# Kernel tuning notes

Hardware: AMD Instinct MI355X
Metric: run time of the kernel (lower is better)

## Reference

```python
import jax, jax.numpy as jnp
import numpy as np

T, K = 2048, 6          # tokens, activated experts per token
DIM = 2048              # model dim
INTER = 1408            # moe intermediate dim
E = 16                  # routed experts (group_size, shared not fused)


def setup_inputs() -> dict:
    key = jax.random.key(0)
    k1, k2, k3, k4, k5, k6 = jax.random.split(key, 6)
    x = jax.random.normal(k1, (T, DIM), dtype=jnp.float32)
    weights = jax.random.uniform(k2, (T, K), dtype=jnp.float32)
    indices = jax.random.randint(k3, (T, K), 0, E, dtype=jnp.int64)
    s = 1.0 / np.sqrt(DIM)
    Wg = jax.random.normal(k4, (E, INTER, DIM), dtype=jnp.float32) * s
    Wu = jax.random.normal(k5, (E, INTER, DIM), dtype=jnp.float32) * s
    Wd = jax.random.normal(k6, (E, DIM, INTER), dtype=jnp.float32) * (1.0 / np.sqrt(INTER))
    return {"x": x, "weights": weights, "indices": indices,
            "Wg": Wg, "Wu": Wu, "Wd": Wd}


def reference(x, weights, indices, Wg, Wu, Wd):
    # per-token combine weight for each expert: [T, E]
    # gate_w[t, e] = sum_k weights[t, k] * (indices[t, k] == e)
    one_hot = jax.nn.one_hot(indices, E, dtype=x.dtype)        # [T, K, E]
    gate_w = jnp.einsum('tk,tke->te', weights, one_hot)        # [T, E]

    # SwiGLU expert FFN, dense over experts, combine folded pre-down-proj
    g = jnp.einsum('td,eid->tei', x, Wg)                       # [T, E, INTER]
    u = jnp.einsum('td,eid->tei', x, Wu)                       # [T, E, INTER]
    act = jax.nn.silu(g) * u                                   # [T, E, INTER]
    # y[t] = sum_e gate_w[t,e] * (act[t,e] @ Wd[e].T)
    y = jnp.einsum('tei,edi->td', act * gate_w[:, :, None], Wd)  # [T, DIM]
    return y
```

## Files before the change

### kernel.cpp

```cpp
#include <hip/hip_runtime.h>
#include <hip/hip_bf16.h>
#include <cstdint>

#define TT     2048
#define KSEL   6
#define DMODEL 2048
#define DINTER 1408
#define NE     16
#define PMAX   (TT * KSEL)

typedef short bf16x8 __attribute__((ext_vector_type(8)));
typedef float f32x4 __attribute__((ext_vector_type(4)));
typedef unsigned short u16;
typedef u16 u16x8 __attribute__((ext_vector_type(8)));

__device__ __forceinline__ u16 f2bf(float f) {
  union { float f; unsigned u; } v; v.f = f;
  return (u16)((v.u + 0x7FFFu + ((v.u >> 16) & 1u)) >> 16);
}
__device__ __forceinline__ float bf2f(u16 h) {
  union { unsigned u; float f; } v; v.u = (unsigned)h << 16; return v.f;
}

__device__ __forceinline__ void gl2lds16(const void* g, void* l) {
  __builtin_amdgcn_global_load_lds((const __attribute__((address_space(1))) void*)g,
                                   (__attribute__((address_space(3))) void*)l,
                                   16, 0, 0);
}

__global__ void k_gate(const float* __restrict__ w, const int* __restrict__ idx,
                       float* __restrict__ gate_w, int* __restrict__ counts) {
  int g = blockIdx.x * 256 + threadIdx.x;
  int t = g >> 4, e = g & 15;
  const int* ip = idx + t * KSEL;
  const float* wp = w + t * KSEL;
  float s = 0.f;
#pragma unroll
  for (int k = 0; k < KSEL; ++k) s += (ip[k] == e) ? wp[k] : 0.f;
  gate_w[g] = s;
  if (s != 0.f) atomicAdd(counts + e, 1);
}

__global__ void k_scan(const int* __restrict__ counts, int* __restrict__ offs) {
  if (threadIdx.x == 0 && blockIdx.x == 0) {
    int r = 0;
#pragma unroll
    for (int e = 0; e < NE; ++e) { offs[e] = r; r += counts[e]; }
    offs[NE] = r;
  }
}

__global__ void k_fill(const float* __restrict__ gate_w, const int* __restrict__ offs,
                       int* __restrict__ cursor, int* __restrict__ slot_tok,
                       float* __restrict__ slot_gate, int* __restrict__ tcnt,
                       int* __restrict__ tok_slots) {
  int g = blockIdx.x * 256 + threadIdx.x;
  int t = g >> 4, e = g & 15;
  float s = gate_w[g];
  if (s != 0.f) {
    int p = atomicAdd(cursor + e, 1);
    int sl = offs[e] + p;
    slot_tok[sl] = t;
    slot_gate[sl] = s;
    int q = atomicAdd(tcnt + t, 1);
    tok_slots[t * KSEL + q] = sl;
  }
}

#define XV8   (TT * DMODEL / 8)
#define WV8   (NE * DINTER * DMODEL / 8)
__global__ void k_cast3(const float* __restrict__ x,  u16* __restrict__ xb,
                        const float* __restrict__ wg, u16* __restrict__ wgb,
                        const float* __restrict__ wu, u16* __restrict__ wub) {
  const int total = XV8 + 2 * WV8;
  int stride = gridDim.x * 256;
  for (int i = blockIdx.x * 256 + threadIdx.x; i < total; i += stride) {
    const float* src; u16* dst; int j;
    if (i < XV8)            { src = x;  dst = xb;  j = i; }
    else if (i < XV8 + WV8) { src = wg; dst = wgb; j = i - XV8; }
    else                    { src = wu; dst = wub; j = i - XV8 - WV8; }
    const float4* p = (const float4*)src + (size_t)j * 2;
    float4 v0 = p[0], v1 = p[1];
    u16x8 o;
    o[0] = f2bf(v0.x); o[1] = f2bf(v0.y); o[2] = f2bf(v0.z); o[3] = f2bf(v0.w);
    o[4] = f2bf(v1.x); o[5] = f2bf(v1.y); o[6] = f2bf(v1.z); o[7] = f2bf(v1.w);
    *(u16x8*)(dst + (size_t)j * 8) = o;
  }
}


__global__ __launch_bounds__(256, 2) void k_gemm1(
    const u16* __restrict__ xb, const u16* __restrict__ wgb, const u16* __restrict__ wub,
    const float* __restrict__ Wd, u16* __restrict__ wdb,
    const int* __restrict__ slot_tok, const float* __restrict__ slot_gate,
    const int* __restrict__ offs, const int* __restrict__ counts,
    u16* __restrict__ act) {
  int bq = blockIdx.x >> 3, br = blockIdx.x & 7;
  if (bq % 5 == 4) {
    int c = (bq / 5) * 8 + br;
    int base = c * 8192;
#pragma unroll 4
    for (int it = 0; it < 32; ++it) {
      int j = base + it * 256 + threadIdx.x;
      const float4* p = (const float4*)Wd + (size_t)j * 2;
      float4 v0 = p[0], v1 = p[1];
      u16x8 o;
      o[0] = f2bf(v0.x); o[1] = f2bf(v0.y); o[2] = f2bf(v0.z); o[3] = f2bf(v0.w);
      o[4] = f2bf(v1.x); o[5] = f2bf(v1.y); o[6] = f2bf(v1.z); o[7] = f2bf(v1.w);
      *(u16x8*)(wdb + (size_t)j * 8) = o;
    }
    return;
  }
  int g = ((bq / 5) * 4 + (bq % 5)) * 8 + br;
  int w = (g & 7) * 352 + (g >> 3);
  int mt = w & 15, rest = w >> 4;
  int it = rest % 11, e = rest / 11;

  int mcount = counts[e];
  if (mt * 128 >= mcount) return;
  int mrem = mcount - mt * 128; if (mrem > 128) mrem = 128;
  int slotBase = offs[e] + mt * 128;
  int iBase = it * 128;

  __shared__ u16 sA[128 * 64];
  __shared__ u16 sG[128 * 64];
  __shared__ u16 sU[128 * 64];
  __shared__ int tokLds[128];
  __shared__ float gateLds[128];

  int tid = threadIdx.x;
  if (tid < 128) {
    int rl = tid < mrem ? tid : 0;
    tokLds[tid] = slot_tok[slotBase + rl];
    gateLds[tid] = (tid < mrem) ? slot_gate[slotBase + rl] : 0.f;
  }
  __syncthreads();

  int wv = tid >> 6, lane = tid & 63;
  const u16 *aSrc[4], *gSrc[4], *uSrc[4];
  u16 *aDst[4], *gDst[4], *uDst[4];
  const u16* gBase = wgb + ((size_t)e * DINTER + iBase) * DMODEL;
  const u16* uBase = wub + ((size_t)e * DINTER + iBase) * DMODEL;
  int r8 = lane >> 3;
  int colOff = ((lane & 7) ^ r8) * 8;
#pragma unroll
  for (int i2 = 0; i2 < 4; ++i2) {
    int chunk = wv * 4 + i2;
    int row = chunk * 8 + r8;
    aSrc[i2] = xb + (size_t)tokLds[row] * DMODEL + colOff;
    gSrc[i2] = gBase + (size_t)row * DMODEL + colOff;
    uSrc[i2] = uBase + (size_t)row * DMODEL + colOff;
    aDst[i2] = sA + chunk * 512;
    gDst[i2] = sG + chunk * 512;
    uDst[i2] = sU + chunk * 512;
  }

  f32x4 accg[4][4] = {};
  f32x4 accu[4][4] = {};
  int fr = lane & 15, fq = lane >> 4;
  int wr = (wv >> 1) * 64, wc = (wv & 1) * 64;

  for (int kb = 0; kb < DMODEL / 64; ++kb) {
    int kOff = kb * 64;
    __syncthreads();
#pragma unroll
    for (int i2 = 0; i2 < 4; ++i2) {
      gl2lds16(aSrc[i2] + kOff, aDst[i2]);
      gl2lds16(gSrc[i2] + kOff, gDst[i2]);
      gl2lds16(uSrc[i2] + kOff, uDst[i2]);
    }
    __syncthreads();
#pragma unroll
    for (int kf = 0; kf < 2; ++kf) {
      bf16x8 af[4], bg[4], bu[4];
#pragma unroll
      for (int mf = 0; mf < 4; ++mf) {
        int row = wr + mf * 16 + fr;
        int cu = ((kf * 4 + fq) ^ (row & 7)) * 8;
        af[mf] = *(const bf16x8*)&sA[row * 64 + cu];
      }
#pragma unroll
      for (int nf = 0; nf < 4; ++nf) {
        int row = wc + nf * 16 + fr;
        int cu = ((kf * 4 + fq) ^ (row & 7)) * 8;
        bg[nf] = *(const bf16x8*)&sG[row * 64 + cu];
        bu[nf] = *(const bf16x8*)&sU[row * 64 + cu];
      }
#pragma unroll
      for (int mf = 0; mf < 4; ++mf)
#pragma unroll
        for (int nf = 0; nf < 4; ++nf) {
          accg[mf][nf] = __builtin_amdgcn_mfma_f32_16x16x32_bf16(af[mf], bg[nf], accg[mf][nf], 0, 0, 0);
          accu[mf][nf] = __builtin_amdgcn_mfma_f32_16x16x32_bf16(af[mf], bu[nf], accu[mf][nf], 0, 0, 0);
        }
    }
  }
#pragma unroll
  for (int mf = 0; mf < 4; ++mf)
#pragma unroll
    for (int nf = 0; nf < 4; ++nf)
#pragma unroll
      for (int r = 0; r < 4; ++r) {
        int row = wr + mf * 16 + fq * 4 + r;
        if (row < mrem) {
          float gv = accg[mf][nf][r], uv = accu[mf][nf][r];
          float a = gv / (1.f + __expf(-gv)) * uv * gateLds[row];
          act[(size_t)(slotBase + row) * DINTER + iBase + wc + nf * 16 + fr] = f2bf(a);
        }
      }
}

__global__ __launch_bounds__(256, 3) void k_gemm2(
    const u16* __restrict__ act, const u16* __restrict__ wdb,
    const int* __restrict__ slot_tok, const int* __restrict__ offs,
    const int* __restrict__ counts, float* __restrict__ y,
    u16* __restrict__ outb) {
  int b = blockIdx.x;
  int w = (b & 7) * 512 + (b >> 3);
  int mt = w & 15, rest = w >> 4;
  int dt = rest & 15, e = rest >> 4;

  int mcount = counts[e];
  if (mt * 128 >= mcount) return;
  int mrem = mcount - mt * 128; if (mrem > 128) mrem = 128;
  int slotBase = offs[e] + mt * 128;
  int dBase = dt * 128;

  __shared__ u16 sA[128 * 64];
  __shared__ u16 sB[128 * 64];
  __shared__ int tokLds[128];

  int tid = threadIdx.x;
  if (tid < 128) tokLds[tid] = slot_tok[slotBase + (tid < mrem ? tid : 0)];
  __syncthreads();

  int wv = tid >> 6, lane = tid & 63;
  const u16 *aSrc[4], *bSrc[4];
  u16 *aDst[4], *bDst[4];
  const u16* bBase = wdb + ((size_t)e * DMODEL + dBase) * DINTER;
  int r8 = lane >> 3;
  int colOff = ((lane & 7) ^ r8) * 8;
#pragma unroll
  for (int i2 = 0; i2 < 4; ++i2) {
    int chunk = wv * 4 + i2;
    int row = chunk * 8 + r8;
    aSrc[i2] = act + (size_t)(slotBase + row) * DINTER + colOff;
    bSrc[i2] = bBase + (size_t)row * DINTER + colOff;
    aDst[i2] = sA + chunk * 512;
    bDst[i2] = sB + chunk * 512;
  }

  f32x4 acc[4][4] = {};
  int fr = lane & 15, fq = lane >> 4;
  int wr = (wv >> 1) * 64, wc = (wv & 1) * 64;

  for (int kb = 0; kb < DINTER / 64; ++kb) {
    int kOff = kb * 64;
    __syncthreads();
#pragma unroll
    for (int i2 = 0; i2 < 4; ++i2) {
      gl2lds16(aSrc[i2] + kOff, aDst[i2]);
      gl2lds16(bSrc[i2] + kOff, bDst[i2]);
    }
    __syncthreads();
#pragma unroll
    for (int kf = 0; kf < 2; ++kf) {
      bf16x8 af[4], bb[4];
#pragma unroll
      for (int mf = 0; mf < 4; ++mf) {
        int row = wr + mf * 16 + fr;
        int cu = ((kf * 4 + fq) ^ (row & 7)) * 8;
        af[mf] = *(const bf16x8*)&sA[row * 64 + cu];
      }
#pragma unroll
      for (int nf = 0; nf < 4; ++nf) {
        int row = wc + nf * 16 + fr;
        int cu = ((kf * 4 + fq) ^ (row & 7)) * 8;
        bb[nf] = *(const bf16x8*)&sB[row * 64 + cu];
      }
#pragma unroll
      for (int mf = 0; mf < 4; ++mf)
#pragma unroll
        for (int nf = 0; nf < 4; ++nf)
          acc[mf][nf] = __builtin_amdgcn_mfma_f32_16x16x32_bf16(af[mf], bb[nf], acc[mf][nf], 0, 0, 0);
    }
  }
#pragma unroll
  for (int mf = 0; mf < 4; ++mf)
#pragma unroll
    for (int nf = 0; nf < 4; ++nf)
#pragma unroll
      for (int r = 0; r < 4; ++r) {
        int row = wr + mf * 16 + fq * 4 + r;
        if (row < mrem) {
          int col = dBase + wc + nf * 16 + fr;
          if (outb) {
            outb[(size_t)(slotBase + row) * DMODEL + col] = f2bf(acc[mf][nf][r]);
          } else {
            atomicAdd(y + (size_t)tokLds[row] * DMODEL + col, acc[mf][nf][r]);
          }
        }
      }
}

__global__ void k_combine(const u16* __restrict__ outb, const int* __restrict__ tok_slots,
                          const int* __restrict__ tcnt, float* __restrict__ y) {
  int idx = blockIdx.x * 256 + threadIdx.x;
  int t = idx >> 8;
  int d0 = (idx & 255) * 8;
  int n = tcnt[t];
  float s[8] = {};
  for (int j = 0; j < n; ++j) {
    int sl = tok_slots[t * KSEL + j];
    u16x8 v = *(const u16x8*)(outb + (size_t)sl * DMODEL + d0);
#pragma unroll
    for (int q = 0; q < 8; ++q) s[q] += bf2f(v[q]);
  }
  float4* yp = (float4*)(y + (size_t)t * DMODEL + d0);
  yp[0] = make_float4(s[0], s[1], s[2], s[3]);
  yp[1] = make_float4(s[4], s[5], s[6], s[7]);
}

extern "C" void kernel_launch(void* const* d_in, const int* in_sizes, int n_in,
                              void* d_out, int out_size, void* d_ws, size_t ws_size,
                              hipStream_t stream) {
  const float* x       = (const float*)d_in[0];
  const float* weights = (const float*)d_in[1];
  const int*   indices = (const int*)d_in[2];
  const float* Wg      = (const float*)d_in[3];
  const float* Wu      = (const float*)d_in[4];
  const float* Wd      = (const float*)d_in[5];
  float* y = (float*)d_out;

  const size_t WELEM = (size_t)NE * DINTER * DMODEL;

  char* ws = (char*)d_ws;
  size_t o = 0;
  float* gate_w = (float*)(ws + o); o += (size_t)TT * NE * 4;
  size_t ctrlOff = o;
  int* counts = (int*)(ws + o);
  int* offs   = (int*)(ws + o + 64);
  int* cursor = (int*)(ws + o + 192);
  int* tcnt   = (int*)(ws + o + 256);
  int* tok_slots = (int*)(ws + o + 256 + TT * 4);
  size_t ctrlZero = 256 + TT * 4;
  o += 256 + TT * 4 + (size_t)TT * KSEL * 4;
  int*   slot_tok  = (int*)(ws + o);   o += (size_t)PMAX * 4;
  float* slot_gate = (float*)(ws + o); o += (size_t)PMAX * 4;
  u16* xb  = (u16*)(ws + o); o += (size_t)TT * DMODEL * 2;
  u16* act = (u16*)(ws + o); o += (size_t)(PMAX + 128) * DINTER * 2;
  u16* wgb = (u16*)(ws + o); o += WELEM * 2;
  u16* wub = (u16*)(ws + o); o += WELEM * 2;
  u16* wdb = (u16*)(ws + o); o += WELEM * 2;
  u16* outb = (u16*)(ws + o);
  size_t oEnd = o + (size_t)PMAX * DMODEL * 2;
  bool useCombine = (ws_size >= oEnd);
  (void)in_sizes; (void)n_in;

  hipMemsetAsync(d_out, 0, (size_t)out_size * 4, stream);
  hipMemsetAsync(ws + ctrlOff, 0, ctrlZero, stream);

  k_gate<<<TT * NE / 256, 256, 0, stream>>>(weights, indices, gate_w, counts);
  k_scan<<<1, 64, 0, stream>>>(counts, offs);
  k_fill<<<TT * NE / 256, 256, 0, stream>>>(gate_w, offs, cursor, slot_tok, slot_gate,
                                            tcnt, tok_slots);
  k_cast3<<<2048, 256, 0, stream>>>(x, xb, Wg, wgb, Wu, wub);
  k_gemm1<<<3520, 256, 0, stream>>>(xb, wgb, wub, Wd, wdb, slot_tok, slot_gate,
                                    offs, counts, act);
  k_gemm2<<<4096, 256, 0, stream>>>(act, wdb, slot_tok, offs, counts, y,
                                    useCombine ? outb : (u16*)nullptr);
  if (useCombine) {
    k_combine<<<TT * DMODEL / 8 / 256, 256, 0, stream>>>(outb, tok_slots, tcnt, y);
  }
}
```

Before: 557.4 us.

## Split gemm1 into two expert halves, overlapping remaining weight casts with compute

The up-front cast kernel now converts only x and the first half of the experts' Wg/Wu to bf16. gemm1 is launched twice, each covering 8 experts. The first launch casts the second half of Wg/Wu in interleaved blocks, and the second launch casts Wd. This hides more of the fp32-to-bf16 conversion traffic behind the GEMM work. The output memset is also skipped when the combine kernel writes y, at the cost of an extra launch and a more intricate block-index mapping.

```diff
diff --git a/kernel.cpp b/kernel.cpp
--- a/kernel.cpp
+++ b/kernel.cpp
@@ -69,16 +69,17 @@
 
 #define XV8   (TT * DMODEL / 8)
 #define WV8   (NE * DINTER * DMODEL / 8)
-__global__ void k_cast3(const float* __restrict__ x,  u16* __restrict__ xb,
-                        const float* __restrict__ wg, u16* __restrict__ wgb,
-                        const float* __restrict__ wu, u16* __restrict__ wub) {
-  const int total = XV8 + 2 * WV8;
+#define WHI   (WV8 / 2)
+__global__ void k_cast_h1(const float* __restrict__ x,  u16* __restrict__ xb,
+                          const float* __restrict__ wg, u16* __restrict__ wgb,
+                          const float* __restrict__ wu, u16* __restrict__ wub) {
+  const int total = XV8 + 2 * WHI;
   int stride = gridDim.x * 256;
   for (int i = blockIdx.x * 256 + threadIdx.x; i < total; i += stride) {
     const float* src; u16* dst; int j;
     if (i < XV8)            { src = x;  dst = xb;  j = i; }
-    else if (i < XV8 + WV8) { src = wg; dst = wgb; j = i - XV8; }
-    else                    { src = wu; dst = wub; j = i - XV8 - WV8; }
+    else if (i < XV8 + WHI) { src = wg; dst = wgb; j = i - XV8; }
+    else                    { src = wu; dst = wub; j = i - XV8 - WHI; }
     const float4* p = (const float4*)src + (size_t)j * 2;
     float4 v0 = p[0], v1 = p[1];
     u16x8 o;
@@ -88,33 +89,36 @@
   }
 }
 
-
 __global__ __launch_bounds__(256, 2) void k_gemm1(
     const u16* __restrict__ xb, const u16* __restrict__ wgb, const u16* __restrict__ wub,
-    const float* __restrict__ Wd, u16* __restrict__ wdb,
+    const float* __restrict__ castS0, u16* __restrict__ castD0, int castO0,
+    const float* __restrict__ castS1, u16* __restrict__ castD1, int castO1,
+    int eBase,
     const int* __restrict__ slot_tok, const float* __restrict__ slot_gate,
     const int* __restrict__ offs, const int* __restrict__ counts,
     u16* __restrict__ act) {
   int bq = blockIdx.x >> 3, br = blockIdx.x & 7;
-  if (bq % 5 == 4) {
-    int c = (bq / 5) * 8 + br;
-    int base = c * 8192;
+  if (bq % 3 == 2) {
+    int c = (bq / 3) * 8 + br;
+    const float* src = (c < 352) ? castS0 : castS1;
+    u16* dst        = (c < 352) ? castD0 : castD1;
+    int base        = ((c < 352) ? castO0 : castO1) + (c % 352) * 8192;
 #pragma unroll 4
     for (int it = 0; it < 32; ++it) {
       int j = base + it * 256 + threadIdx.x;
-      const float4* p = (const float4*)Wd + (size_t)j * 2;
+      const float4* p = (const float4*)src + (size_t)j * 2;
       float4 v0 = p[0], v1 = p[1];
       u16x8 o;
       o[0] = f2bf(v0.x); o[1] = f2bf(v0.y); o[2] = f2bf(v0.z); o[3] = f2bf(v0.w);
       o[4] = f2bf(v1.x); o[5] = f2bf(v1.y); o[6] = f2bf(v1.z); o[7] = f2bf(v1.w);
-      *(u16x8*)(wdb + (size_t)j * 8) = o;
+      *(u16x8*)(dst + (size_t)j * 8) = o;
     }
     return;
   }
-  int g = ((bq / 5) * 4 + (bq % 5)) * 8 + br;
-  int w = (g & 7) * 352 + (g >> 3);
+  int g = ((bq / 3) * 2 + (bq % 3)) * 8 + br;
+  int w = (g & 7) * 176 + (g >> 3);
   int mt = w & 15, rest = w >> 4;
-  int it = rest % 11, e = rest / 11;
+  int it = rest % 11, e = eBase + rest / 11;
 
   int mcount = counts[e];
   if (mt * 128 >= mcount) return;
@@ -333,6 +337,7 @@
   float* y = (float*)d_out;
 
   const size_t WELEM = (size_t)NE * DINTER * DMODEL;
+  const int HOFF = (int)WHI;
 
   char* ws = (char*)d_ws;
   size_t o = 0;
@@ -357,16 +362,20 @@
   bool useCombine = (ws_size >= oEnd);
   (void)in_sizes; (void)n_in;
 
-  hipMemsetAsync(d_out, 0, (size_t)out_size * 4, stream);
+  if (!useCombine) hipMemsetAsync(d_out, 0, (size_t)out_size * 4, stream);
   hipMemsetAsync(ws + ctrlOff, 0, ctrlZero, stream);
 
   k_gate<<<TT * NE / 256, 256, 0, stream>>>(weights, indices, gate_w, counts);
   k_scan<<<1, 64, 0, stream>>>(counts, offs);
   k_fill<<<TT * NE / 256, 256, 0, stream>>>(gate_w, offs, cursor, slot_tok, slot_gate,
                                             tcnt, tok_slots);
-  k_cast3<<<2048, 256, 0, stream>>>(x, xb, Wg, wgb, Wu, wub);
-  k_gemm1<<<3520, 256, 0, stream>>>(xb, wgb, wub, Wd, wdb, slot_tok, slot_gate,
-                                    offs, counts, act);
+  k_cast_h1<<<2048, 256, 0, stream>>>(x, xb, Wg, wgb, Wu, wub);
+  k_gemm1<<<2112, 256, 0, stream>>>(xb, wgb, wub,
+                                    Wg, wgb, HOFF, Wu, wub, HOFF, 0,
+                                    slot_tok, slot_gate, offs, counts, act);
+  k_gemm1<<<2112, 256, 0, stream>>>(xb, wgb, wub,
+                                    Wd, wdb, 0, Wd, wdb, HOFF, 8,
+                                    slot_tok, slot_gate, offs, counts, act);
   k_gemm2<<<4096, 256, 0, stream>>>(act, wdb, slot_tok, offs, counts, y,
                                     useCombine ? outb : (u16*)nullptr);
   if (useCombine) {
```

After: 575.0 us. 1.03x slower.
